# Optimization experiments

Hardware: AMD Instinct MI355X
Metric: run time of the kernel (lower is better)

The kernel has to match this reference:

```python
import jax, jax.numpy as jnp
import numpy as np

N = 100_000   # nodes
E = 6_400_000  # edges (avg degree 64)
K = 3          # TAGConv hops -> K+1 linear terms per layer


def setup_inputs() -> dict:
    key = jax.random.key(0)
    ks = jax.random.split(key, 9)
    return {
        "x": jax.random.normal(ks[0], (N,), jnp.float32),
        "edge_index": jax.random.randint(ks[1], (2, E), 0, N, jnp.int32),
        "edge_attr": jax.random.normal(ks[2], (E,), jnp.float32),
        "k": 5000,
        "W1": jax.random.normal(ks[3], (K + 1, 1, 8), jnp.float32) * 0.5,
        "b1": jax.random.normal(ks[4], (8,), jnp.float32) * 0.1,
        "W2": jax.random.normal(ks[5], (K + 1, 8, 8), jnp.float32) * 0.2,
        "b2": jax.random.normal(ks[6], (8,), jnp.float32) * 0.1,
        "W3": jax.random.normal(ks[7], (K + 1, 8, 1), jnp.float32) * 0.2,
        "b3": jax.random.normal(ks[8], (1,), jnp.float32) * 0.1,
    }


def _gcn_norm(src, dst, edge_weight, num_nodes):
    # PyG gcn_norm with add_self_loops=False: deg over target index,
    # norm_e = d^{-1/2}[src] * w_e * d^{-1/2}[dst]
    deg = jax.ops.segment_sum(edge_weight, dst, num_segments=num_nodes)
    dis = jnp.where(deg > 0, jax.lax.rsqrt(jnp.where(deg > 0, deg, 1.0)), 0.0)
    return dis[src] * edge_weight * dis[dst]


def _tagconv(x, W, b, src, dst, norm, num_nodes):
    # out = sum_{h=0..K} (A_norm^h x) @ W[h] + b
    out = x @ W[0]
    h = x
    for i in range(1, W.shape[0]):
        h = jax.ops.segment_sum(norm[:, None] * h[src], dst, num_segments=num_nodes)
        out = out + h @ W[i]
    return out + b


def reference(x, edge_index, edge_attr, k, W1, b1, W2, b2, W3, b3):
    num_nodes = x.shape[0]
    x = x[:, None]  # [N, 1]
    src, dst = edge_index[0], edge_index[1]
    norm = _gcn_norm(src, dst, jnp.abs(edge_attr), num_nodes)

    x = jax.nn.relu(_tagconv(x, W1, b1, src, dst, norm, num_nodes))
    x = jax.nn.relu(_tagconv(x, W2, b2, src, dst, norm, num_nodes))
    x = jax.nn.relu(_tagconv(x, W3, b3, src, dst, norm, num_nodes))

    # tg.nn.InstanceNorm(1), batch=None, affine=False: normalize over all nodes
    mean = jnp.mean(x)
    var = jnp.mean((x - mean) ** 2)
    x = ((x - mean) * jax.lax.rsqrt(var + 1e-5)).squeeze(-1)  # [N]

    # top-k one-hot mask (argsort descending -> first k indices)
    _, top_idx = jax.lax.top_k(x, k)
    top_vec = jnp.zeros_like(x).at[top_idx].set(1.0)
    return jnp.column_stack((x, top_vec))  # [N, 2]
```

## Files before the change

kernel.cpp:

```cpp
#include <hip/hip_runtime.h>

#define BS 256
#define GPN 16
#define NBLKB 1024
#define BSH 8

static __device__ __forceinline__ float relu_(float v) { return fmaxf(v, 0.0f); }


__global__ void k_binhist(const int* __restrict__ dst, int* __restrict__ bcnt,
                          int E, int chunk, int nbuck) {
  __shared__ int h[1024];
  int b = blockIdx.x, t = threadIdx.x;
  for (int i = t; i < nbuck; i += BS) h[i] = 0;
  __syncthreads();
  int beg = b * chunk, end = min(E, beg + chunk);
  for (int e = beg + t; e < end; e += BS) atomicAdd(&h[dst[e] >> BSH], 1);
  __syncthreads();
  for (int i = t; i < nbuck; i += BS) bcnt[(size_t)i * NBLKB + b] = h[i];
}

__global__ void k_bucketscan(int* __restrict__ bcnt, int* __restrict__ btot) {
  __shared__ int sh[BS];
  int bkt = blockIdx.x, t = threadIdx.x;
  size_t base = (size_t)bkt * NBLKB;
  int c[4], s = 0;
#pragma unroll
  for (int j = 0; j < 4; ++j) { c[j] = bcnt[base + t * 4 + j]; s += c[j]; }
  sh[t] = s; __syncthreads();
  for (int off = 1; off < BS; off <<= 1) {
    int add = (t >= off) ? sh[t - off] : 0; __syncthreads();
    sh[t] += add; __syncthreads();
  }
  int run = sh[t] - s;
#pragma unroll
  for (int j = 0; j < 4; ++j) { bcnt[base + t * 4 + j] = run; run += c[j]; }
  if (t == BS - 1) btot[bkt] = run;
}

__global__ void k_basescan(const int* __restrict__ btot, int* __restrict__ bbase, int nbuck) {
  __shared__ int sh[BS];
  int t = threadIdx.x;
  int run = 0;
  for (int c = 0; c < nbuck; c += BS) {
    int i = c + t;
    int v = (i < nbuck) ? btot[i] : 0;
    sh[t] = v; __syncthreads();
    for (int off = 1; off < BS; off <<= 1) {
      int add = (t >= off) ? sh[t - off] : 0; __syncthreads();
      sh[t] += add; __syncthreads();
    }
    if (i < nbuck) bbase[i] = run + sh[t] - v;
    run += sh[BS - 1];
    __syncthreads();
  }
}

__global__ void k_bin(const int* __restrict__ src, const int* __restrict__ dst,
                      const float* __restrict__ attr, const int* __restrict__ bcnt,
                      const int* __restrict__ bbase, int2* __restrict__ bed,
                      int E, int chunk, int nbuck) {
  __shared__ int cur[1024];
  int b = blockIdx.x, t = threadIdx.x;
  for (int i = t; i < nbuck; i += BS)
    cur[i] = bbase[i] + bcnt[(size_t)i * NBLKB + b];
  __syncthreads();
  int beg = b * chunk, end = min(E, beg + chunk);
  for (int e = beg + t; e < end; e += BS) {
    int d = dst[e];
    int bkt = d >> BSH;
    int pos = atomicAdd(&cur[bkt], 1);
    unsigned packed = ((unsigned)(d & ((1 << BSH) - 1)) << 17) | (unsigned)src[e];
    bed[pos] = make_int2((int)packed, __float_as_int(fabsf(attr[e])));
  }
}

__global__ void k_cntdeg(const int2* __restrict__ bed, const int* __restrict__ bbase,
                         const int* __restrict__ btot, const float* __restrict__ x,
                         int* __restrict__ cnt, float* __restrict__ dis,
                         float* __restrict__ xhat, int N) {
  __shared__ int   lc[1 << BSH];
  __shared__ float ld[1 << BSH];
  int bkt = blockIdx.x, t = threadIdx.x;
  for (int i = t; i < (1 << BSH); i += BS) { lc[i] = 0; ld[i] = 0.f; }
  __syncthreads();
  int beg = bbase[bkt], tot = btot[bkt];
  for (int i = t; i < tot; i += BS) {
    int2 rec = bed[beg + i];
    int dl = (int)((unsigned)rec.x >> 17);
    atomicAdd(&lc[dl], 1);
    atomicAdd(&ld[dl], __int_as_float(rec.y));
  }
  __syncthreads();
  int nb = bkt << BSH;
  for (int i = t; i < (1 << BSH); i += BS) {
    int n = nb + i;
    if (n < N) {
      cnt[n] = lc[i];
      float dg = ld[i];
      float d = (dg > 0.f) ? (1.0f / sqrtf(dg)) : 0.f;
      dis[n] = d;
      xhat[n] = d * x[n];
    }
  }
}

__global__ void k_fill(const int2* __restrict__ bed, const int* __restrict__ bbase,
                       const int* __restrict__ btot, const int* __restrict__ rowptr,
                       int2* __restrict__ adj, int N) {
  __shared__ int rcur[1 << BSH];
  int bkt = blockIdx.x, t = threadIdx.x;
  int nb = bkt << BSH;
  for (int i = t; i < (1 << BSH); i += BS) {
    int n = nb + i;
    rcur[i] = (n < N) ? rowptr[n] : 0;
  }
  __syncthreads();
  int beg = bbase[bkt], tot = btot[bkt];
  for (int i = t; i < tot; i += BS) {
    int2 rec = bed[beg + i];
    unsigned u = (unsigned)rec.x;
    int dl = (int)(u >> 17);
    int s  = (int)(u & 0x1FFFFu);
    int pos = atomicAdd(&rcur[dl], 1);
    adj[pos] = make_int2(s, rec.y);
  }
}


__global__ void k_scanA(const int* __restrict__ cnt, int* __restrict__ bsum, int N) {
  __shared__ int sh[BS];
  int t = threadIdx.x;
  int base = blockIdx.x * 1024;
  int s = 0;
#pragma unroll
  for (int j = 0; j < 4; ++j) { int i = base + t * 4 + j; s += (i < N) ? cnt[i] : 0; }
  sh[t] = s; __syncthreads();
  for (int off = 128; off; off >>= 1) { if (t < off) sh[t] += sh[t + off]; __syncthreads(); }
  if (t == 0) bsum[blockIdx.x] = sh[0];
}

__global__ void k_scanB(int* __restrict__ bsum, int NB2) {
  __shared__ int sh[BS];
  int t = threadIdx.x;
  int v = (t < NB2) ? bsum[t] : 0;
  sh[t] = v; __syncthreads();
  for (int off = 1; off < BS; off <<= 1) {
    int add = (t >= off) ? sh[t - off] : 0; __syncthreads();
    sh[t] += add; __syncthreads();
  }
  if (t < NB2) bsum[t] = sh[t] - v;
}

__global__ void k_scanC(const int* __restrict__ cnt, const int* __restrict__ bsum,
                        int* __restrict__ rowptr, int* __restrict__ cursor, int N, int E) {
  __shared__ int sh[BS];
  int b = blockIdx.x, t = threadIdx.x;
  int base = b * 1024;
  int c[4]; int s = 0;
#pragma unroll
  for (int j = 0; j < 4; ++j) { int i = base + t * 4 + j; c[j] = (i < N) ? cnt[i] : 0; s += c[j]; }
  sh[t] = s; __syncthreads();
  for (int off = 1; off < BS; off <<= 1) {
    int add = (t >= off) ? sh[t - off] : 0; __syncthreads();
    sh[t] += add; __syncthreads();
  }
  int run = sh[t] - s + bsum[b];
#pragma unroll
  for (int j = 0; j < 4; ++j) {
    int i = base + t * 4 + j;
    if (i < N) { rowptr[i] = run; if (cursor) cursor[i] = run; run += c[j]; }
  }
  if (b == 0 && t == 0) rowptr[N] = E;
}


__global__ void k_count(const int* __restrict__ dst, int* __restrict__ cnt, int E) {
  int e = blockIdx.x * blockDim.x + threadIdx.x;
  if (e < E) atomicAdd(&cnt[dst[e]], 1);
}

__global__ void k_place(const int* __restrict__ src, const int* __restrict__ dst,
                        const float* __restrict__ attr, int* __restrict__ cursor,
                        int2* __restrict__ adj, int E) {
  int e = blockIdx.x * blockDim.x + threadIdx.x;
  if (e >= E) return;
  int d = dst[e];
  int pos = atomicAdd(&cursor[d], 1);
  adj[pos] = make_int2(src[e], __float_as_int(fabsf(attr[e])));
}

__global__ void k_degdis(const int* __restrict__ rowptr, const int2* __restrict__ adj,
                         const float* __restrict__ x, float* __restrict__ dis,
                         float* __restrict__ xhat, int N) {
  int g = (blockIdx.x * blockDim.x + threadIdx.x) / GPN;
  int l = threadIdx.x & (GPN - 1);
  if (g >= N) return;
  int beg = rowptr[g], end = rowptr[g + 1];
  float s = 0.0f;
  for (int e = beg + l; e < end; e += GPN) s += __int_as_float(adj[e].y);
#pragma unroll
  for (int off = 8; off; off >>= 1) s += __shfl_xor(s, off, GPN);
  if (l == 0) {
    float d = (s > 0.0f) ? (1.0f / sqrtf(s)) : 0.0f;
    dis[g] = d;
    xhat[g] = d * x[g];
  }
}


__global__ void k_gp1_uh(const int* __restrict__ rowptr, const int2* __restrict__ adj,
                         const float* __restrict__ uin, const float* __restrict__ dis,
                         float* __restrict__ hout, float* __restrict__ uout, int N) {
  int g = (blockIdx.x * blockDim.x + threadIdx.x) / GPN;
  int l = threadIdx.x & (GPN - 1);
  if (g >= N) return;
  int beg = rowptr[g], end = rowptr[g + 1];
  float acc = 0.0f;
  for (int e = beg + l; e < end; e += GPN) {
    int2 sw = adj[e];
    acc += __int_as_float(sw.y) * uin[sw.x];
  }
#pragma unroll
  for (int off = 8; off; off >>= 1) acc += __shfl_xor(acc, off, GPN);
  if (l == 0) {
    float d = dis[g];
    float h = d * acc;
    hout[g] = h;
    uout[g] = d * h;
  }
}

__global__ void k_gp1_y(const int* __restrict__ rowptr, const int2* __restrict__ adj,
                        const float* __restrict__ u2, const float* __restrict__ x,
                        const float* __restrict__ h1, const float* __restrict__ h2,
                        const float* __restrict__ dis, const float* __restrict__ W1,
                        const float* __restrict__ b1, const float* __restrict__ W23,
                        float* __restrict__ y, float* __restrict__ Phat, int N) {
  int g = (blockIdx.x * blockDim.x + threadIdx.x) / GPN;
  int l = threadIdx.x & (GPN - 1);
  if (g >= N) return;
  int beg = rowptr[g], end = rowptr[g + 1];
  float acc = 0.0f;
  for (int e = beg + l; e < end; e += GPN) {
    int2 sw = adj[e];
    acc += __int_as_float(sw.y) * u2[sw.x];
  }
#pragma unroll
  for (int off = 8; off; off >>= 1) acc += __shfl_xor(acc, off, GPN);
  if (l == 0) {
    float d = dis[g];
    float xv = x[g], a = h1[g], b = h2[g], c = d * acc;
    float o[8];
#pragma unroll
    for (int j = 0; j < 8; ++j)
      o[j] = relu_(xv * W1[j] + a * W1[8 + j] + b * W1[16 + j] + c * W1[24 + j] + b1[j]);
    float4* op = (float4*)(y + (size_t)g * 8);
    op[0] = make_float4(o[0], o[1], o[2], o[3]);
    op[1] = make_float4(o[4], o[5], o[6], o[7]);
    float p[8];
#pragma unroll
    for (int j = 0; j < 8; ++j) {
      float s = 0.0f;
#pragma unroll
      for (int i = 0; i < 8; ++i) s += o[i] * W23[i * 8 + j];
      p[j] = d * s;
    }
    float4* pp = (float4*)(Phat + (size_t)g * 8);
    pp[0] = make_float4(p[0], p[1], p[2], p[3]);
    pp[1] = make_float4(p[4], p[5], p[6], p[7]);
  }
}

__global__ void k_gp8_u(const int* __restrict__ rowptr, const int2* __restrict__ adj,
                        const float* __restrict__ uin, const float* __restrict__ y,
                        const float* __restrict__ W, const float* __restrict__ dis,
                        float* __restrict__ uout, int N) {
  int g = (blockIdx.x * blockDim.x + threadIdx.x) / GPN;
  int l = threadIdx.x & (GPN - 1);
  if (g >= N) return;
  int beg = rowptr[g], end = rowptr[g + 1];
  float a0=0,a1=0,a2=0,a3=0,a4=0,a5=0,a6=0,a7=0;
  for (int e = beg + l; e < end; e += GPN) {
    int2 sw = adj[e];
    float w = __int_as_float(sw.y);
    const float4* hp = (const float4*)(uin + (size_t)sw.x * 8);
    float4 u = hp[0], v = hp[1];
    a0 += w*u.x; a1 += w*u.y; a2 += w*u.z; a3 += w*u.w;
    a4 += w*v.x; a5 += w*v.y; a6 += w*v.z; a7 += w*v.w;
  }
#pragma unroll
  for (int off = 8; off; off >>= 1) {
    a0 += __shfl_xor(a0, off, GPN); a1 += __shfl_xor(a1, off, GPN);
    a2 += __shfl_xor(a2, off, GPN); a3 += __shfl_xor(a3, off, GPN);
    a4 += __shfl_xor(a4, off, GPN); a5 += __shfl_xor(a5, off, GPN);
    a6 += __shfl_xor(a6, off, GPN); a7 += __shfl_xor(a7, off, GPN);
  }
  if (l == 0) {
    float d = dis[g];
    const float4* yp = (const float4*)(y + (size_t)g * 8);
    float4 u = yp[0], v = yp[1];
    float yi[8] = {u.x, u.y, u.z, u.w, v.x, v.y, v.z, v.w};
    float acc[8] = {a0, a1, a2, a3, a4, a5, a6, a7};
    float o[8];
#pragma unroll
    for (int j = 0; j < 8; ++j) {
      float s = 0.0f;
#pragma unroll
      for (int i = 0; i < 8; ++i) s += yi[i] * W[i * 8 + j];
      o[j] = d * (s + d * acc[j]);
    }
    float4* op = (float4*)(uout + (size_t)g * 8);
    op[0] = make_float4(o[0], o[1], o[2], o[3]);
    op[1] = make_float4(o[4], o[5], o[6], o[7]);
  }
}

__global__ void k_gp8_fin(const int* __restrict__ rowptr, const int2* __restrict__ adj,
                          const float* __restrict__ uin, const float* __restrict__ y,
                          const float* __restrict__ W0, const float* __restrict__ b2,
                          const float* __restrict__ W3, const float* __restrict__ dis,
                          float* __restrict__ S3hat, float* __restrict__ B2,
                          float* __restrict__ B1, float* __restrict__ B0, int N) {
  int g = (blockIdx.x * blockDim.x + threadIdx.x) / GPN;
  int l = threadIdx.x & (GPN - 1);
  if (g >= N) return;
  int beg = rowptr[g], end = rowptr[g + 1];
  float a0=0,a1=0,a2=0,a3=0,a4=0,a5=0,a6=0,a7=0;
  for (int e = beg + l; e < end; e += GPN) {
    int2 sw = adj[e];
    float w = __int_as_float(sw.y);
    const float4* hp = (const float4*)(uin + (size_t)sw.x * 8);
    float4 u = hp[0], v = hp[1];
    a0 += w*u.x; a1 += w*u.y; a2 += w*u.z; a3 += w*u.w;
    a4 += w*v.x; a5 += w*v.y; a6 += w*v.z; a7 += w*v.w;
  }
#pragma unroll
  for (int off = 8; off; off >>= 1) {
    a0 += __shfl_xor(a0, off, GPN); a1 += __shfl_xor(a1, off, GPN);
    a2 += __shfl_xor(a2, off, GPN); a3 += __shfl_xor(a3, off, GPN);
    a4 += __shfl_xor(a4, off, GPN); a5 += __shfl_xor(a5, off, GPN);
    a6 += __shfl_xor(a6, off, GPN); a7 += __shfl_xor(a7, off, GPN);
  }
  if (l == 0) {
    float d = dis[g];
    const float4* yp = (const float4*)(y + (size_t)g * 8);
    float4 u = yp[0], v = yp[1];
    float yi[8] = {u.x, u.y, u.z, u.w, v.x, v.y, v.z, v.w};
    float acc[8] = {a0, a1, a2, a3, a4, a5, a6, a7};
    float z[8];
#pragma unroll
    for (int j = 0; j < 8; ++j) {
      float s = 0.0f;
#pragma unroll
      for (int i = 0; i < 8; ++i) s += yi[i] * W0[i * 8 + j];
      z[j] = relu_(s + d * acc[j] + b2[j]);
    }
    float t[4];
#pragma unroll
    for (int i = 0; i < 4; ++i) {
      float s = 0.0f;
#pragma unroll
      for (int j = 0; j < 8; ++j) s += z[j] * W3[i * 8 + j];
      t[i] = s;
    }
    B0[g] = t[0]; B1[g] = t[1]; B2[g] = t[2];
    S3hat[g] = d * t[3];
  }
}

__global__ void k_gp1_bu(const int* __restrict__ rowptr, const int2* __restrict__ adj,
                         const float* __restrict__ uin, const float* __restrict__ B,
                         const float* __restrict__ dis, float* __restrict__ uout, int N) {
  int g = (blockIdx.x * blockDim.x + threadIdx.x) / GPN;
  int l = threadIdx.x & (GPN - 1);
  if (g >= N) return;
  int beg = rowptr[g], end = rowptr[g + 1];
  float acc = 0.0f;
  for (int e = beg + l; e < end; e += GPN) {
    int2 sw = adj[e];
    acc += __int_as_float(sw.y) * uin[sw.x];
  }
#pragma unroll
  for (int off = 8; off; off >>= 1) acc += __shfl_xor(acc, off, GPN);
  if (l == 0) {
    float d = dis[g];
    uout[g] = d * (B[g] + d * acc);
  }
}

__global__ void k_gp1_last(const int* __restrict__ rowptr, const int2* __restrict__ adj,
                           const float* __restrict__ uin, const float* __restrict__ B0,
                           const float* __restrict__ b3, const float* __restrict__ dis,
                           float* __restrict__ r, unsigned* __restrict__ keys,
                           double* __restrict__ partials, int N) {
  __shared__ double s1[BS];
  __shared__ double s2[BS];
  int tid = blockIdx.x * blockDim.x + threadIdx.x;
  int g = tid / GPN, l = tid & (GPN - 1);
  float rv = 0.0f;
  bool writer = false;
  if (g < N) {
    int beg = rowptr[g], end = rowptr[g + 1];
    float acc = 0.0f;
    for (int e = beg + l; e < end; e += GPN) {
      int2 sw = adj[e];
      acc += __int_as_float(sw.y) * uin[sw.x];
    }
#pragma unroll
    for (int off = 8; off; off >>= 1) acc += __shfl_xor(acc, off, GPN);
    if (l == 0) {
      float gg = B0[g] + dis[g] * acc;
      rv = relu_(gg + b3[0]);
      r[g] = rv;
      keys[g] = __float_as_uint(rv) | 0x80000000u;
      writer = true;
    }
  }
  double v = writer ? (double)rv : 0.0;
  s1[threadIdx.x] = v;
  s2[threadIdx.x] = v * v;
  __syncthreads();
  for (int off = 128; off; off >>= 1) {
    if (threadIdx.x < off) {
      s1[threadIdx.x] += s1[threadIdx.x + off];
      s2[threadIdx.x] += s2[threadIdx.x + off];
    }
    __syncthreads();
  }
  if (threadIdx.x == 0) {
    partials[2 * (size_t)blockIdx.x]     = s1[0];
    partials[2 * (size_t)blockIdx.x + 1] = s2[0];
  }
}

__global__ void k_stats(const double* __restrict__ partials, int nparts,
                        float* __restrict__ stats, int N) {
  __shared__ double s1[BS];
  __shared__ double s2[BS];
  int t = threadIdx.x;
  double a = 0.0, b = 0.0;
  for (int i = t; i < nparts; i += BS) { a += partials[2 * (size_t)i]; b += partials[2 * (size_t)i + 1]; }
  s1[t] = a; s2[t] = b;
  __syncthreads();
  for (int off = 128; off; off >>= 1) {
    if (t < off) { s1[t] += s1[t + off]; s2[t] += s2[t + off]; }
    __syncthreads();
  }
  if (t == 0) {
    double mean = s1[0] / (double)N;
    double var  = s2[0] / (double)N - mean * mean;
    stats[0] = (float)mean;
    stats[1] = (float)(1.0 / sqrt(var + 1e-5));
  }
}


__global__ void k_stateinit(unsigned* __restrict__ state, const int* __restrict__ kp) {
  state[0] = 0u;
  state[1] = (unsigned)kp[0];
}

__global__ void k_hist(const unsigned* __restrict__ keys, int N,
                       const unsigned* __restrict__ state, unsigned* __restrict__ hist,
                       int shift) {
  __shared__ unsigned sh[256];
  sh[threadIdx.x] = 0;
  __syncthreads();
  unsigned prefix = state[0];
  unsigned hmask = (shift >= 24) ? 0u : (0xFFFFFFFFu << (shift + 8));
  int stride = gridDim.x * blockDim.x;
  for (int n = blockIdx.x * blockDim.x + threadIdx.x; n < N; n += stride) {
    unsigned kk = keys[n];
    if ((kk & hmask) == (prefix & hmask)) atomicAdd(&sh[(kk >> shift) & 255u], 1u);
  }
  __syncthreads();
  atomicAdd(&hist[threadIdx.x], sh[threadIdx.x]);
}

__global__ void k_select(unsigned* __restrict__ state, unsigned* __restrict__ hist, int shift) {
  __shared__ unsigned sh[BS];
  int t = threadIdx.x;
  unsigned c = hist[t];
  sh[t] = c;
  __syncthreads();
  for (int off = 1; off < BS; off <<= 1) {
    unsigned add = (t + off < BS) ? sh[t + off] : 0u; __syncthreads();
    sh[t] += add; __syncthreads();
  }
  unsigned rem = state[1];
  unsigned S = sh[t];
  if (S >= rem && (S - c) < rem) {
    state[0] |= ((unsigned)t) << shift;
    state[1] = rem - (S - c);
  }
  hist[t] = 0;
}

__global__ void k_mark(const unsigned* __restrict__ keys, const float* __restrict__ r,
                       const float* __restrict__ stats, int N,
                       const unsigned* __restrict__ state, float* __restrict__ out,
                       unsigned* __restrict__ blkcnt) {
  unsigned T = state[0];
  float mean = stats[0], istd = stats[1];
  int n = blockIdx.x * 256 + threadIdx.x;
  int eq = 0;
  __shared__ int sh;
  if (threadIdx.x == 0) sh = 0;
  __syncthreads();
  if (n < N) {
    out[2 * (size_t)n] = (r[n] - mean) * istd;
    unsigned kk = keys[n];
    out[2 * (size_t)n + 1] = (kk > T) ? 1.0f : 0.0f;
    eq = (kk == T);
  }
  if (eq) atomicAdd(&sh, 1);
  __syncthreads();
  if (threadIdx.x == 0) blkcnt[blockIdx.x] = (unsigned)sh;
}

__global__ void k_scanP(const unsigned* __restrict__ blkcnt, unsigned* __restrict__ scanbuf, int NB) {
  __shared__ unsigned sh[BS];
  int t = threadIdx.x;
  unsigned c0 = (2 * t < NB) ? blkcnt[2 * t] : 0u;
  unsigned c1 = (2 * t + 1 < NB) ? blkcnt[2 * t + 1] : 0u;
  unsigned s = c0 + c1;
  sh[t] = s; __syncthreads();
  for (int off = 1; off < BS; off <<= 1) {
    unsigned add = (t >= off) ? sh[t - off] : 0u; __syncthreads();
    sh[t] += add; __syncthreads();
  }
  unsigned ex = sh[t] - s;
  if (2 * t < NB) scanbuf[2 * t] = ex;
  if (2 * t + 1 < NB) scanbuf[2 * t + 1] = ex + c0;
}

__global__ void k_resolve(const unsigned* __restrict__ keys, int N,
                          const unsigned* __restrict__ state,
                          const unsigned* __restrict__ scanbuf, float* __restrict__ out) {
  unsigned T = state[0];
  unsigned m = state[1];
  int n = blockIdx.x * 256 + threadIdx.x;
  if (n >= N) return;
  if (keys[n] != T) return;
  unsigned rank = scanbuf[blockIdx.x];
  int base = blockIdx.x * 256;
  for (int j = base; j < n; ++j) rank += (keys[j] == T);
  out[2 * (size_t)n + 1] = (rank < m) ? 1.0f : 0.0f;
}


extern "C" void kernel_launch(void* const* d_in, const int* in_sizes, int n_in,
                              void* d_out, int out_size, void* d_ws, size_t ws_size,
                              hipStream_t stream) {
  const float* x    = (const float*)d_in[0];
  const int*   ei   = (const int*)d_in[1];
  const float* attr = (const float*)d_in[2];
  const int*   kp   = (const int*)d_in[3];
  const float* W1   = (const float*)d_in[4];
  const float* b1   = (const float*)d_in[5];
  const float* W2   = (const float*)d_in[6];
  const float* b2   = (const float*)d_in[7];
  const float* W3   = (const float*)d_in[8];
  const float* b3   = (const float*)d_in[9];
  const int N = in_sizes[0];
  const int E = in_sizes[2];
  const int* src = ei;
  const int* dst = ei + E;
  float* out = (float*)d_out;
  const int NB    = (N + 255) / 256;
  const int NB2   = (N + 1023) / 1024;
  const int NBUCK = (N + (1 << BSH) - 1) >> BSH;
  const int chunk = (E + NBLKB - 1) / NBLKB;
  const int GGB   = (int)(((size_t)N * GPN + BS - 1) / BS);

  char* p = (char*)d_ws;
  auto alloc = [&](size_t bytes) -> char* {
    char* r = p; p += (bytes + 255) & ~(size_t)255; return r;
  };
  float*    dis    = (float*)alloc((size_t)N * 4);
  float*    xhat   = (float*)alloc((size_t)N * 4);
  float*    h1     = (float*)alloc((size_t)N * 4);
  float*    h2     = (float*)alloc((size_t)N * 4);
  float*    u1     = (float*)alloc((size_t)N * 4);
  float*    u2     = (float*)alloc((size_t)N * 4);
  float*    y      = (float*)alloc((size_t)N * 32);
  float*    Phat   = (float*)alloc((size_t)N * 32);
  float*    Qhat   = (float*)alloc((size_t)N * 32);
  float*    S3hat  = (float*)alloc((size_t)N * 4);
  float*    B2     = (float*)alloc((size_t)N * 4);
  float*    B1     = (float*)alloc((size_t)N * 4);
  float*    B0     = (float*)alloc((size_t)N * 4);
  float*    g2hat  = (float*)alloc((size_t)N * 4);
  float*    g1hat  = (float*)alloc((size_t)N * 4);
  float*    r      = (float*)alloc((size_t)N * 4);
  unsigned* keys   = (unsigned*)alloc((size_t)N * 4);
  double*   parts  = (double*)alloc((size_t)GGB * 16);
  float*    stats  = (float*)alloc(8);
  unsigned* state  = (unsigned*)alloc(8);
  unsigned* hist   = (unsigned*)alloc(1024);
  unsigned* blkcnt = (unsigned*)alloc((size_t)NB * 4);
  unsigned* scanbf = (unsigned*)alloc((size_t)NB * 4);
  int*      rowptr = (int*)alloc((size_t)(N + 1) * 4);
  int*      cursor = (int*)alloc((size_t)N * 4);
  int*      cnt    = (int*)alloc((size_t)N * 4);
  int*      bsum   = (int*)alloc(2048);
  int2*     adj    = (int2*)alloc((size_t)E * 8);
  size_t need_mid = (size_t)(p - (char*)d_ws);
  int2*     bed    = (int2*)alloc((size_t)E * 8);
  int*      bcnt   = (int*)alloc((size_t)NBUCK * NBLKB * 4);
  int*      btot   = (int*)alloc((size_t)NBUCK * 4 + 256);
  int*      bbase  = (int*)alloc((size_t)NBUCK * 4 + 256);
  size_t need_new = (size_t)(p - (char*)d_ws);

  dim3 B(BS);
  int genb = (E + BS - 1) / BS;
  dim3 GE(genb), GG(GGB), GN(NB), GB(NBUCK);

  bool use_new = (need_new <= ws_size) && (N <= 131072) && (NBUCK <= 1024);

  hipMemsetAsync(hist, 0, 1024, stream);

  if (use_new) {
    k_binhist<<<dim3(NBLKB), B, 0, stream>>>(dst, bcnt, E, chunk, NBUCK);
    k_bucketscan<<<GB, B, 0, stream>>>(bcnt, btot);
    k_basescan<<<dim3(1), B, 0, stream>>>(btot, bbase, NBUCK);
    k_bin<<<dim3(NBLKB), B, 0, stream>>>(src, dst, attr, bcnt, bbase, bed, E, chunk, NBUCK);
    k_cntdeg<<<GB, B, 0, stream>>>(bed, bbase, btot, x, cnt, dis, xhat, N);
    k_scanA<<<dim3(NB2), B, 0, stream>>>(cnt, bsum, N);
    k_scanB<<<dim3(1), B, 0, stream>>>(bsum, NB2);
    k_scanC<<<dim3(NB2), B, 0, stream>>>(cnt, bsum, rowptr, (int*)nullptr, N, E);
    k_fill<<<GB, B, 0, stream>>>(bed, bbase, btot, rowptr, adj, N);
  } else {
    hipMemsetAsync(cnt, 0, (size_t)N * 4, stream);
    k_count<<<GE, B, 0, stream>>>(dst, cnt, E);
    k_scanA<<<dim3(NB2), B, 0, stream>>>(cnt, bsum, N);
    k_scanB<<<dim3(1), B, 0, stream>>>(bsum, NB2);
    k_scanC<<<dim3(NB2), B, 0, stream>>>(cnt, bsum, rowptr, cursor, N, E);
    k_place<<<GE, B, 0, stream>>>(src, dst, attr, cursor, adj, E);
    k_degdis<<<GG, B, 0, stream>>>(rowptr, adj, x, dis, xhat, N);
  }

  k_gp1_uh<<<GG, B, 0, stream>>>(rowptr, adj, xhat, dis, h1, u1, N);
  k_gp1_uh<<<GG, B, 0, stream>>>(rowptr, adj, u1, dis, h2, u2, N);
  k_gp1_y<<<GG, B, 0, stream>>>(rowptr, adj, u2, x, h1, h2, dis, W1, b1, W2 + 3 * 64, y, Phat, N);

  k_gp8_u<<<GG, B, 0, stream>>>(rowptr, adj, Phat, y, W2 + 2 * 64, dis, Qhat, N);
  k_gp8_u<<<GG, B, 0, stream>>>(rowptr, adj, Qhat, y, W2 + 1 * 64, dis, Phat, N);
  k_gp8_fin<<<GG, B, 0, stream>>>(rowptr, adj, Phat, y, W2, b2, W3, dis, S3hat, B2, B1, B0, N);

  k_gp1_bu<<<GG, B, 0, stream>>>(rowptr, adj, S3hat, B2, dis, g2hat, N);
  k_gp1_bu<<<GG, B, 0, stream>>>(rowptr, adj, g2hat, B1, dis, g1hat, N);
  k_gp1_last<<<GG, B, 0, stream>>>(rowptr, adj, g1hat, B0, b3, dis, r, keys, parts, N);

  k_stats<<<dim3(1), B, 0, stream>>>(parts, GGB, stats, N);

  k_stateinit<<<dim3(1), dim3(1), 0, stream>>>(state, kp);
  for (int shift = 24; shift >= 0; shift -= 8) {
    k_hist<<<GN, B, 0, stream>>>(keys, N, state, hist, shift);
    k_select<<<dim3(1), B, 0, stream>>>(state, hist, shift);
  }
  k_mark<<<GN, B, 0, stream>>>(keys, r, stats, N, state, out, blkcnt);
  k_scanP<<<dim3(1), B, 0, stream>>>(blkcnt, scanbf, NB);
  k_resolve<<<GN, B, 0, stream>>>(keys, N, state, scanbf, out);
}
```

Baseline: 615.3 us.

## Stage bin/fill scatter writes in shared memory and fuse rowptr scan into cntdeg

```diff
diff --git a/kernel.cpp b/kernel.cpp
--- a/kernel.cpp
+++ b/kernel.cpp
@@ -4,6 +4,7 @@
 #define GPN 16
 #define NBLKB 1024
 #define BSH 8
+#define SMAX 400
 
 static __device__ __forceinline__ float relu_(float v) { return fmaxf(v, 0.0f); }
 
@@ -60,29 +61,57 @@
                       const float* __restrict__ attr, const int* __restrict__ bcnt,
                       const int* __restrict__ bbase, int2* __restrict__ bed,
                       int E, int chunk, int nbuck) {
-  __shared__ int cur[1024];
+  __shared__ int2 stage[SMAX][8];
+  __shared__ int  fc[SMAX];
+  __shared__ int  cur[SMAX];
   int b = blockIdx.x, t = threadIdx.x;
-  for (int i = t; i < nbuck; i += BS)
+  for (int i = t; i < nbuck; i += BS) {
     cur[i] = bbase[i] + bcnt[(size_t)i * NBLKB + b];
+    fc[i] = 0;
+  }
   __syncthreads();
   int beg = b * chunk, end = min(E, beg + chunk);
-  for (int e = beg + t; e < end; e += BS) {
-    int d = dst[e];
-    int bkt = d >> BSH;
-    int pos = atomicAdd(&cur[bkt], 1);
-    unsigned packed = ((unsigned)(d & ((1 << BSH) - 1)) << 17) | (unsigned)src[e];
-    bed[pos] = make_int2((int)packed, __float_as_int(fabsf(attr[e])));
+  for (int base = beg; base < end; base += BS) {
+    int e = base + t;
+    if (e < end) {
+      int d = dst[e];
+      int bkt = d >> BSH;
+      int2 rec = make_int2((int)(((unsigned)(d & ((1 << BSH) - 1)) << 17) | (unsigned)src[e]),
+                           __float_as_int(fabsf(attr[e])));
+      int slot = atomicAdd(&fc[bkt], 1);
+      if (slot < 8) stage[bkt][slot] = rec;
+      else { int gp = atomicAdd(&cur[bkt], 1); bed[gp] = rec; }
+    }
+    __syncthreads();
+    for (int i = t; i < nbuck; i += BS) {
+      int c = fc[i]; if (c > 8) c = 8;
+      if (c == 8) {
+        int gp = cur[i]; cur[i] = gp + 8;
+#pragma unroll
+        for (int j = 0; j < 8; ++j) bed[gp + j] = stage[i][j];
+        fc[i] = 0;
+      }
+    }
+    __syncthreads();
+  }
+  for (int i = t; i < nbuck; i += BS) {
+    int c = fc[i]; if (c > 8) c = 8;
+    if (c) {
+      int gp = cur[i];
+      for (int j = 0; j < c; ++j) bed[gp + j] = stage[i][j];
+    }
   }
 }
 
 __global__ void k_cntdeg(const int2* __restrict__ bed, const int* __restrict__ bbase,
                          const int* __restrict__ btot, const float* __restrict__ x,
-                         int* __restrict__ cnt, float* __restrict__ dis,
-                         float* __restrict__ xhat, int N) {
+                         float* __restrict__ dis, float* __restrict__ xhat,
+                         int* __restrict__ rowptr, int N, int E) {
   __shared__ int   lc[1 << BSH];
   __shared__ float ld[1 << BSH];
+  __shared__ int   sc[1 << BSH];
   int bkt = blockIdx.x, t = threadIdx.x;
-  for (int i = t; i < (1 << BSH); i += BS) { lc[i] = 0; ld[i] = 0.f; }
+  lc[t] = 0; ld[t] = 0.f;
   __syncthreads();
   int beg = bbase[bkt], tot = btot[bkt];
   for (int i = t; i < tot; i += BS) {
@@ -92,38 +121,65 @@
     atomicAdd(&ld[dl], __int_as_float(rec.y));
   }
   __syncthreads();
-  int nb = bkt << BSH;
-  for (int i = t; i < (1 << BSH); i += BS) {
-    int n = nb + i;
-    if (n < N) {
-      cnt[n] = lc[i];
-      float dg = ld[i];
-      float d = (dg > 0.f) ? (1.0f / sqrtf(dg)) : 0.f;
-      dis[n] = d;
-      xhat[n] = d * x[n];
-    }
-  }
+  int c = lc[t];
+  sc[t] = c;
+  __syncthreads();
+  for (int off = 1; off < BS; off <<= 1) {
+    int add = (t >= off) ? sc[t - off] : 0; __syncthreads();
+    sc[t] += add; __syncthreads();
+  }
+  int n = (bkt << BSH) + t;
+  if (n < N) {
+    rowptr[n] = beg + sc[t] - c;
+    float dg = ld[t];
+    float d = (dg > 0.f) ? (1.0f / sqrtf(dg)) : 0.f;
+    dis[n] = d;
+    xhat[n] = d * x[n];
+  }
+  if (t == 0 && bkt == (int)gridDim.x - 1) rowptr[N] = E;
 }
 
 __global__ void k_fill(const int2* __restrict__ bed, const int* __restrict__ bbase,
                        const int* __restrict__ btot, const int* __restrict__ rowptr,
                        int2* __restrict__ adj, int N) {
-  __shared__ int rcur[1 << BSH];
+  __shared__ int2 stage[1 << BSH][8];
+  __shared__ int  fc[1 << BSH];
+  __shared__ int  rcur[1 << BSH];
   int bkt = blockIdx.x, t = threadIdx.x;
-  int nb = bkt << BSH;
-  for (int i = t; i < (1 << BSH); i += BS) {
-    int n = nb + i;
-    rcur[i] = (n < N) ? rowptr[n] : 0;
-  }
+  int n = (bkt << BSH) + t;
+  rcur[t] = (n < N) ? rowptr[n] : 0;
+  fc[t] = 0;
   __syncthreads();
   int beg = bbase[bkt], tot = btot[bkt];
-  for (int i = t; i < tot; i += BS) {
-    int2 rec = bed[beg + i];
-    unsigned u = (unsigned)rec.x;
-    int dl = (int)(u >> 17);
-    int s  = (int)(u & 0x1FFFFu);
-    int pos = atomicAdd(&rcur[dl], 1);
-    adj[pos] = make_int2(s, rec.y);
+  for (int base = 0; base < tot; base += BS) {
+    int i = base + t;
+    if (i < tot) {
+      int2 rec = bed[beg + i];
+      unsigned u = (unsigned)rec.x;
+      int dl = (int)(u >> 17);
+      int2 orec = make_int2((int)(u & 0x1FFFFu), rec.y);
+      int slot = atomicAdd(&fc[dl], 1);
+      if (slot < 8) stage[dl][slot] = orec;
+      else { int gp = atomicAdd(&rcur[dl], 1); adj[gp] = orec; }
+    }
+    __syncthreads();
+    {
+      int c = fc[t]; if (c > 8) c = 8;
+      if (c == 8) {
+        int gp = rcur[t]; rcur[t] = gp + 8;
+#pragma unroll
+        for (int j = 0; j < 8; ++j) adj[gp + j] = stage[t][j];
+        fc[t] = 0;
+      }
+    }
+    __syncthreads();
+  }
+  {
+    int c = fc[t]; if (c > 8) c = 8;
+    if (c) {
+      int gp = rcur[t];
+      for (int j = 0; j < c; ++j) adj[gp + j] = stage[t][j];
+    }
   }
 }
 
@@ -617,7 +673,7 @@
   int genb = (E + BS - 1) / BS;
   dim3 GE(genb), GG(GGB), GN(NB), GB(NBUCK);
 
-  bool use_new = (need_new <= ws_size) && (N <= 131072) && (NBUCK <= 1024);
+  bool use_new = (need_new <= ws_size) && (N <= 131072) && (NBUCK <= SMAX);
 
   hipMemsetAsync(hist, 0, 1024, stream);
 
@@ -626,10 +682,7 @@
     k_bucketscan<<<GB, B, 0, stream>>>(bcnt, btot);
     k_basescan<<<dim3(1), B, 0, stream>>>(btot, bbase, NBUCK);
     k_bin<<<dim3(NBLKB), B, 0, stream>>>(src, dst, attr, bcnt, bbase, bed, E, chunk, NBUCK);
-    k_cntdeg<<<GB, B, 0, stream>>>(bed, bbase, btot, x, cnt, dis, xhat, N);
-    k_scanA<<<dim3(NB2), B, 0, stream>>>(cnt, bsum, N);
-    k_scanB<<<dim3(1), B, 0, stream>>>(bsum, NB2);
-    k_scanC<<<dim3(NB2), B, 0, stream>>>(cnt, bsum, rowptr, (int*)nullptr, N, E);
+    k_cntdeg<<<GB, B, 0, stream>>>(bed, bbase, btot, x, dis, xhat, rowptr, N, E);
     k_fill<<<GB, B, 0, stream>>>(bed, bbase, btot, rowptr, adj, N);
   } else {
     hipMemsetAsync(cnt, 0, (size_t)N * 4, stream);
```

After: 581.9 us. 5.4% less time.
